# Kernel tuning notes

Measured on AMD Instinct MI355X. Metric: run time of the kernel, lower is better.

Reference implementation:

```python
import jax, jax.numpy as jnp
import numpy as np

HOPS = 3


def setup_inputs() -> dict:
    key = jax.random.key(0)
    ks = jax.random.split(key, 16)
    B, S, H, P = 8, 256, 768, 256
    N_E, N_T, N_R, T_TOK = 20000, 100000, 200, 4
    inv = H ** -0.5
    return {
        "last_hidden_state": jax.random.normal(ks[0], (B, S, H), jnp.float32),
        "attn_mask": jnp.ones((B, S), jnp.float32),
        "init_ent": jax.random.uniform(ks[1], (B, N_E), jnp.float32),
        "ents_embeds": jax.random.normal(ks[2], (N_E, T_TOK, H), jnp.float32) * 0.02,
        "W_q": jax.random.normal(ks[3], (H, P), jnp.float32) * inv,
        "W_v": jax.random.normal(ks[4], (H, P), jnp.float32) * inv,
        "W_p": jax.random.normal(ks[5], (P, 1), jnp.float32) * (P ** -0.5),
        "W_r": jax.random.normal(ks[6], (H, HOPS * N_R), jnp.float32) * inv,
        "W_c": jax.random.normal(ks[7], (H, HOPS * 2), jnp.float32) * inv,
        "L_w": jax.random.normal(ks[8], (H, H), jnp.float32) * inv,
        "heads": jax.random.randint(ks[9], (B, N_T), 0, N_E, jnp.int32),
        "rels": jax.random.randint(ks[10], (B, N_T), 0, N_R, jnp.int32),
        "tails": jax.random.randint(ks[11], (B, N_T), 0, N_E, jnp.int32),
    }


def reference(last_hidden_state, attn_mask, init_ent, ents_embeds,
              W_q, W_v, W_p, W_r, W_c, L_w, heads, rels, tails):
    B, S, H = last_hidden_state.shape
    N_E = init_ent.shape[1]

    # --- _pointer + _pointer_vecs: pointer attention over dialogue tokens ---
    D0 = last_hidden_state[:, -1, :]                                  # (B,H) last token = dialogue repr
    logits = (jnp.einsum('bh,hp->bp', D0, W_q)[:, None, :]
              + jnp.einsum('bsh,hp->bsp', last_hidden_state, W_v))    # (B,S,P)
    pointers = jax.nn.softmax(jnp.einsum('bsp,p->bs', logits, W_p[:, 0]), axis=1)
    D = jnp.sum(pointers[:, :, None] * last_hidden_state * attn_mask[:, :, None], axis=1)  # (B,H)

    # --- predict_rels / predict_checks ---
    rels_seq = jax.nn.softmax((D @ W_r).reshape(B, HOPS, -1), axis=2)    # (B,hops,N_R)
    checks_seq = jax.nn.softmax((D @ W_c).reshape(B, HOPS, -1), axis=2)  # (B,hops,2)

    # --- NEXT: per-batch per-hop sparse KG walk, one-hot sparse mm == gather/scatter ---
    def walk_one(e0, r_seq, h_idx, r_idx, t_idx):
        def hop(e, r):
            trip = r[r_idx] * e[h_idx]                                   # (N_T,) per-triple mass
            walked = jax.ops.segment_sum(trip, t_idx, num_segments=N_E)  # scatter to tails
            walked = walked / (walked.sum() + 1e-6)
            return walked, walked
        _, es = jax.lax.scan(hop, e0, r_seq)
        return es                                                        # (hops,N_E)

    walk = jax.vmap(walk_one)(init_ent, rels_seq, heads, rels, tails)    # (B,hops,N_E)

    # --- operates_on_checks: broadcasted matmul reduces to a single dot per (b,e) ---
    LD = D @ L_w                                                         # (B,H)
    scores = jnp.einsum('bh,eth->be', LD, ents_embeds)                   # (B,N_E)
    checks = jax.nn.softmax(walk * scores[:, None, :], axis=-1)          # (B,hops,N_E)

    # --- walk_or_check: mix walk vs check distribution per hop ---
    combined = jnp.stack([walk, checks], axis=2)                         # (B,hops,2,N_E)
    ents = jnp.einsum('bhc,bhce->bhe', checks_seq, combined)             # (B,hops,N_E)
    return ents
```

## Files before the change

### kernel.cpp

```cpp
#include <hip/hip_runtime.h>
#include <math.h>

#define NB 8
#define NS 256
#define NH 768
#define NE 20000
#define NT 100000

__device__ __forceinline__ float wsum(float v) {
#pragma unroll
  for (int off = 32; off; off >>= 1) v += __shfl_xor(v, off, 64);
  return v;
}
__device__ __forceinline__ float wmax(float v) {
#pragma unroll
  for (int off = 32; off; off >>= 1) v = fmaxf(v, __shfl_xor(v, off, 64));
  return v;
}

__global__ void k_prep(const float* __restrict__ Wv, const float* __restrict__ Wp,
                       float* __restrict__ wv) {
  int wave = threadIdx.x >> 6, lane = threadIdx.x & 63;
  int h = blockIdx.x * 4 + wave;
  const float4* Wv4 = (const float4*)Wv;
  const float4* Wp4 = (const float4*)Wp;
  float4 a = Wv4[h * 64 + lane];
  float4 p = Wp4[lane];
  float v = a.x * p.x + a.y * p.y + a.z * p.z + a.w * p.w;
  v = wsum(v);
  if (lane == 0) wv[h] = v;
}

__global__ void k_score(const float* __restrict__ lhs, const float* __restrict__ wv,
                        float* __restrict__ score) {
  int chunk = blockIdx.x, b = blockIdx.y;
  int wave = threadIdx.x >> 6, lane = threadIdx.x & 63;
  const float4* lhs4 = (const float4*)lhs;
  const float4* wv4 = (const float4*)wv;
  float4 w0 = wv4[lane], w1 = wv4[lane + 64], w2 = wv4[lane + 128];
#pragma unroll
  for (int i = 0; i < 8; i++) {
    int s = chunk * 32 + i * 4 + wave;
    const float4* row = lhs4 + (size_t)(b * NS + s) * 192;
    float4 a0 = row[lane], a1 = row[lane + 64], a2 = row[lane + 128];
    float v = a0.x * w0.x + a0.y * w0.y + a0.z * w0.z + a0.w * w0.w
            + a1.x * w1.x + a1.y * w1.y + a1.z * w1.z + a1.w * w1.w
            + a2.x * w2.x + a2.y * w2.y + a2.z * w2.z + a2.w * w2.w;
    v = wsum(v);
    if (lane == 0) score[b * NS + s] = v;
  }
}

__global__ void k_D(const float* __restrict__ lhs, const float* __restrict__ mask,
                    const float* __restrict__ score, float* __restrict__ Dv) {
  int b = blockIdx.x, chunk = blockIdx.y;
  int tid = threadIdx.x;
  __shared__ float red[256];
  __shared__ float pm[NS];
  float sv = score[b * NS + tid];
  red[tid] = sv; __syncthreads();
  for (int st = 128; st; st >>= 1) {
    if (tid < st) red[tid] = fmaxf(red[tid], red[tid + st]);
    __syncthreads();
  }
  float M = red[0]; __syncthreads();
  float e = expf(sv - M);
  red[tid] = e; __syncthreads();
  for (int st = 128; st; st >>= 1) {
    if (tid < st) red[tid] += red[tid + st];
    __syncthreads();
  }
  float Ssum = red[0];
  pm[tid] = (e / Ssum) * mask[b * NS + tid];
  __syncthreads();
  int h = chunk * 256 + tid;
  float acc = 0.f;
#pragma unroll 4
  for (int s = 0; s < NS; s++) acc += pm[s] * lhs[(size_t)(b * NS + s) * NH + h];
  Dv[b * NH + h] = acc;
}

__global__ void k_small(const float* __restrict__ Dv, const float* __restrict__ Wr,
                        const float* __restrict__ Wc, const float* __restrict__ Lw,
                        float* __restrict__ rels_raw, float* __restrict__ checks_raw,
                        float* __restrict__ LD) {
  __shared__ float Dl[NB * NH];
  __shared__ float part[4][64][8];
  int tid = threadIdx.x;
  for (int i = tid; i < NB * NH; i += 256) Dl[i] = Dv[i];
  __syncthreads();
  int c = tid & 63, q = tid >> 6;
  int C = blockIdx.x * 64 + c;
  const float* Wb = nullptr;
  float* outp = nullptr;
  int stride = 0, ostride = 0, col = 0;
  bool valid = (C < 1374);
  if (C < 600)      { Wb = Wr; stride = 600; col = C;       outp = rels_raw;   ostride = 600; }
  else if (C < 606) { Wb = Wc; stride = 6;   col = C - 600; outp = checks_raw; ostride = 6; }
  else if (valid)   { Wb = Lw; stride = 768; col = C - 606; outp = LD;         ostride = 768; }
  float p[8] = {0, 0, 0, 0, 0, 0, 0, 0};
  if (valid) {
    int h0 = q * 192;
    for (int h = h0; h < h0 + 192; h++) {
      float w = Wb[(size_t)h * stride + col];
#pragma unroll
      for (int b = 0; b < 8; b++) p[b] += Dl[b * NH + h] * w;
    }
  }
#pragma unroll
  for (int b = 0; b < 8; b++) part[q][c][b] = p[b];
  __syncthreads();
  if (q == 0 && valid) {
    for (int b = 0; b < 8; b++) {
      float v = part[0][c][b] + part[1][c][b] + part[2][c][b] + part[3][c][b];
      outp[b * ostride + col] = v;
    }
  }
}

__global__ void k_small2(float* __restrict__ rels, float* __restrict__ checks) {
  int b = blockIdx.x;
  int hop = threadIdx.x >> 6, lane = threadIdx.x & 63;
  float* r = rels + (size_t)(b * 3 + hop) * 200;
  float v0 = r[lane], v1 = r[lane + 64], v2 = r[lane + 128];
  float v3 = (lane < 8) ? r[lane + 192] : -INFINITY;
  float m = wmax(fmaxf(fmaxf(v0, v1), fmaxf(v2, v3)));
  float e0 = expf(v0 - m), e1 = expf(v1 - m), e2 = expf(v2 - m);
  float e3 = (lane < 8) ? expf(v3 - m) : 0.f;
  float s = wsum(e0 + e1 + e2 + e3);
  r[lane] = e0 / s; r[lane + 64] = e1 / s; r[lane + 128] = e2 / s;
  if (lane < 8) r[lane + 192] = e3 / s;
  if (lane == 0) {
    float* cc = checks + b * 6 + hop * 2;
    float c0 = cc[0], c1 = cc[1];
    float mm = fmaxf(c0, c1);
    float f0 = expf(c0 - mm), f1 = expf(c1 - mm);
    cc[0] = f0 / (f0 + f1); cc[1] = f1 / (f0 + f1);
  }
}

__global__ __launch_bounds__(256) void k_scores(const float* __restrict__ EE,
                                                const float* __restrict__ LD,
                                                float* __restrict__ scores) {
  int wave = threadIdx.x >> 6, lane = threadIdx.x & 63;
  int e = blockIdx.x * 4 + wave;
  const float4* EE4 = (const float4*)EE;
  const float4* LD4 = (const float4*)LD;
  float4 ld[3][8];
#pragma unroll
  for (int ph = 0; ph < 3; ph++)
#pragma unroll
    for (int b = 0; b < 8; b++) ld[ph][b] = LD4[b * 192 + ph * 64 + lane];
  float acc[8] = {0, 0, 0, 0, 0, 0, 0, 0};
  const float4* base = EE4 + (size_t)e * 768 + lane;
#pragma unroll
  for (int k = 0; k < 12; k++) {
    float4 v = base[k * 64];
    const int ph = k % 3;
#pragma unroll
    for (int b = 0; b < 8; b++)
      acc[b] += v.x * ld[ph][b].x + v.y * ld[ph][b].y + v.z * ld[ph][b].z + v.w * ld[ph][b].w;
  }
#pragma unroll
  for (int off = 32; off; off >>= 1)
#pragma unroll
    for (int b = 0; b < 8; b++) acc[b] += __shfl_xor(acc[b], off, 64);
  if (lane == 0) {
#pragma unroll
    for (int b = 0; b < 8; b++) scores[b * NE + e] = acc[b];
  }
}

__global__ void k_scatter(const int* __restrict__ heads, const int* __restrict__ rels,
                          const int* __restrict__ tails, const float* __restrict__ rels_seq,
                          const float* __restrict__ init_ent, const float* __restrict__ walk,
                          float* __restrict__ acc, int hop) {
  int t = blockIdx.x * 256 + threadIdx.x;
  if (t >= NB * NT) return;
  int b = t / NT;
  int hi = heads[t], ri = rels[t], ti = tails[t];
  float ev = (hop == 0) ? init_ent[(size_t)b * NE + hi]
                        : walk[((size_t)(b * 3) + hop - 1) * NE + hi];
  float rv = rels_seq[(size_t)(b * 3 + hop) * 200 + ri];
  atomicAdd(&acc[(size_t)b * NE + ti], rv * ev);
}

__global__ void k_norm(float* __restrict__ acc, float* __restrict__ walk, int hop) {
  int b = blockIdx.x, tid = threadIdx.x;
  float s = 0.f;
  for (int e = tid; e < NE; e += 1024) s += acc[(size_t)b * NE + e];
  s = wsum(s);
  __shared__ float red[16];
  __shared__ float stot;
  if ((tid & 63) == 0) red[tid >> 6] = s;
  __syncthreads();
  if (tid == 0) {
    float tt = 0.f;
    for (int i = 0; i < 16; i++) tt += red[i];
    stot = tt + 1e-6f;
  }
  __syncthreads();
  float denom = stot;
  float* w = walk + (size_t)(b * 3 + hop) * NE;
  for (int e = tid; e < NE; e += 1024) {
    w[e] = acc[(size_t)b * NE + e] / denom;
    acc[(size_t)b * NE + e] = 0.f;
  }
}

__global__ void k_final(const float* __restrict__ walk, const float* __restrict__ scores,
                        const float* __restrict__ checks_seq, float* __restrict__ out) {
  int row = blockIdx.x;
  int b = row / 3, hop = row % 3;
  const float* w = walk + (size_t)row * NE;
  const float* sc = scores + (size_t)b * NE;
  int tid = threadIdx.x;
  __shared__ float red[4];
  __shared__ float MM, SS;
  float m = -INFINITY;
  for (int e = tid; e < NE; e += 256) m = fmaxf(m, w[e] * sc[e]);
  m = wmax(m);
  if ((tid & 63) == 0) red[tid >> 6] = m;
  __syncthreads();
  if (tid == 0) MM = fmaxf(fmaxf(red[0], red[1]), fmaxf(red[2], red[3]));
  __syncthreads();
  float M = MM;
  float s = 0.f;
  for (int e = tid; e < NE; e += 256) s += expf(w[e] * sc[e] - M);
  s = wsum(s);
  if ((tid & 63) == 0) red[tid >> 6] = s;
  __syncthreads();
  if (tid == 0) SS = red[0] + red[1] + red[2] + red[3];
  __syncthreads();
  float Sv = SS;
  float cs0 = checks_seq[b * 6 + hop * 2 + 0];
  float cs1 = checks_seq[b * 6 + hop * 2 + 1];
  for (int e = tid; e < NE; e += 256) {
    float we = w[e];
    out[(size_t)row * NE + e] = cs0 * we + cs1 * (expf(we * sc[e] - M) / Sv);
  }
}

extern "C" void kernel_launch(void* const* d_in, const int* in_sizes, int n_in,
                              void* d_out, int out_size, void* d_ws, size_t ws_size,
                              hipStream_t stream) {
  const float* lhs      = (const float*)d_in[0];
  const float* mask     = (const float*)d_in[1];
  const float* init_ent = (const float*)d_in[2];
  const float* EE       = (const float*)d_in[3];
  const float* Wv       = (const float*)d_in[5];
  const float* Wp       = (const float*)d_in[6];
  const float* Wr       = (const float*)d_in[7];
  const float* Wc       = (const float*)d_in[8];
  const float* Lw       = (const float*)d_in[9];
  const int* heads      = (const int*)d_in[10];
  const int* rels       = (const int*)d_in[11];
  const int* tails      = (const int*)d_in[12];
  float* out = (float*)d_out;
  float* ws = (float*)d_ws;

  float* wv         = ws + 0;
  float* score      = ws + 768;
  float* Dv         = ws + 2816;
  float* LD         = ws + 8960;
  float* rels_seq   = ws + 15104;
  float* checks_seq = ws + 19904;
  float* scores     = ws + 19952;
  float* acc        = ws + 179952;
  float* walk       = ws + 339952;

  hipMemsetAsync(acc, 0, (size_t)NB * NE * sizeof(float), stream);
  k_prep<<<192, 256, 0, stream>>>(Wv, Wp, wv);
  k_score<<<dim3(8, NB), 256, 0, stream>>>(lhs, wv, score);
  k_D<<<dim3(NB, 3), 256, 0, stream>>>(lhs, mask, score, Dv);
  k_small<<<22, 256, 0, stream>>>(Dv, Wr, Wc, Lw, rels_seq, checks_seq, LD);
  k_small2<<<NB, 192, 0, stream>>>(rels_seq, checks_seq);
  k_scores<<<5000, 256, 0, stream>>>(EE, LD, scores);
  for (int hop = 0; hop < 3; hop++) {
    k_scatter<<<(NB * NT + 255) / 256, 256, 0, stream>>>(heads, rels, tails, rels_seq,
                                                         init_ent, walk, acc, hop);
    k_norm<<<NB, 1024, 0, stream>>>(acc, walk, hop);
  }
  k_final<<<NB * 3, 256, 0, stream>>>(walk, scores, checks_seq, out);
}
```

Baseline: 684.3 us.

## Fuse KG walk hops into one per-batch kernel with LDS atomics

Replaces the three scatter+normalize launch pairs and the global accumulator memset with a single kernel. Each of the 8 blocks holds its batch's 20000-entry accumulator in shared memory and runs all three hops with LDS atomics instead of global atomics. The pointer-softmax kernel now does its reduction with wave shuffles and splits the sequence sum across 4 thread groups, and the final softmax kernel uses 1024 threads per row. The walk now runs on only 8 workgroups, so the scatter has far less parallelism and relies on shared-memory atomics being fast enough to compensate.

```diff
diff --git a/kernel.cpp b/kernel.cpp
--- a/kernel.cpp
+++ b/kernel.cpp
@@ -51,33 +51,37 @@
   }
 }
 
-__global__ void k_D(const float* __restrict__ lhs, const float* __restrict__ mask,
-                    const float* __restrict__ score, float* __restrict__ Dv) {
+__global__ __launch_bounds__(1024) void k_D(const float* __restrict__ lhs,
+                                            const float* __restrict__ mask,
+                                            const float* __restrict__ score,
+                                            float* __restrict__ Dv) {
   int b = blockIdx.x, chunk = blockIdx.y;
   int tid = threadIdx.x;
-  __shared__ float red[256];
   __shared__ float pm[NS];
-  float sv = score[b * NS + tid];
-  red[tid] = sv; __syncthreads();
-  for (int st = 128; st; st >>= 1) {
-    if (tid < st) red[tid] = fmaxf(red[tid], red[tid + st]);
-    __syncthreads();
-  }
-  float M = red[0]; __syncthreads();
-  float e = expf(sv - M);
-  red[tid] = e; __syncthreads();
-  for (int st = 128; st; st >>= 1) {
-    if (tid < st) red[tid] += red[tid + st];
-    __syncthreads();
-  }
-  float Ssum = red[0];
-  pm[tid] = (e / Ssum) * mask[b * NS + tid];
-  __syncthreads();
-  int h = chunk * 256 + tid;
+  __shared__ float part[4][256];
+  if (tid < 64) {
+    int lane = tid;
+    float v0 = score[b * NS + lane], v1 = score[b * NS + lane + 64];
+    float v2 = score[b * NS + lane + 128], v3 = score[b * NS + lane + 192];
+    float m = wmax(fmaxf(fmaxf(v0, v1), fmaxf(v2, v3)));
+    float e0 = expf(v0 - m), e1 = expf(v1 - m), e2 = expf(v2 - m), e3 = expf(v3 - m);
+    float s = wsum(e0 + e1 + e2 + e3);
+    pm[lane] = e0 / s * mask[b * NS + lane];
+    pm[lane + 64] = e1 / s * mask[b * NS + lane + 64];
+    pm[lane + 128] = e2 / s * mask[b * NS + lane + 128];
+    pm[lane + 192] = e3 / s * mask[b * NS + lane + 192];
+  }
+  __syncthreads();
+  int g = tid >> 8;
+  int hh = tid & 255;
+  int h = chunk * 256 + hh;
   float acc = 0.f;
-#pragma unroll 4
-  for (int s = 0; s < NS; s++) acc += pm[s] * lhs[(size_t)(b * NS + s) * NH + h];
-  Dv[b * NH + h] = acc;
+  const float* base = lhs + (size_t)(b * NS + g * 64) * NH + h;
+#pragma unroll 8
+  for (int s = 0; s < 64; s++) acc += pm[g * 64 + s] * base[(size_t)s * NH];
+  part[g][hh] = acc;
+  __syncthreads();
+  if (g == 0) Dv[b * NH + h] = part[0][hh] + part[1][hh] + part[2][hh] + part[3][hh];
 }
 
 __global__ void k_small(const float* __restrict__ Dv, const float* __restrict__ Wr,
@@ -171,71 +175,94 @@
   }
 }
 
-__global__ void k_scatter(const int* __restrict__ heads, const int* __restrict__ rels,
-                          const int* __restrict__ tails, const float* __restrict__ rels_seq,
-                          const float* __restrict__ init_ent, const float* __restrict__ walk,
-                          float* __restrict__ acc, int hop) {
-  int t = blockIdx.x * 256 + threadIdx.x;
-  if (t >= NB * NT) return;
-  int b = t / NT;
-  int hi = heads[t], ri = rels[t], ti = tails[t];
-  float ev = (hop == 0) ? init_ent[(size_t)b * NE + hi]
-                        : walk[((size_t)(b * 3) + hop - 1) * NE + hi];
-  float rv = rels_seq[(size_t)(b * 3 + hop) * 200 + ri];
-  atomicAdd(&acc[(size_t)b * NE + ti], rv * ev);
-}
-
-__global__ void k_norm(float* __restrict__ acc, float* __restrict__ walk, int hop) {
-  int b = blockIdx.x, tid = threadIdx.x;
-  float s = 0.f;
-  for (int e = tid; e < NE; e += 1024) s += acc[(size_t)b * NE + e];
-  s = wsum(s);
+__global__ __launch_bounds__(1024) void k_walk(const int* __restrict__ heads,
+                                               const int* __restrict__ rels,
+                                               const int* __restrict__ tails,
+                                               const float* __restrict__ rels_seq,
+                                               const float* __restrict__ init_ent,
+                                               float* __restrict__ walk) {
+  int b = blockIdx.x;
+  int tid = threadIdx.x;
+  __shared__ float accs[NE];
   __shared__ float red[16];
   __shared__ float stot;
-  if ((tid & 63) == 0) red[tid >> 6] = s;
-  __syncthreads();
-  if (tid == 0) {
-    float tt = 0.f;
-    for (int i = 0; i < 16; i++) tt += red[i];
-    stot = tt + 1e-6f;
-  }
-  __syncthreads();
-  float denom = stot;
-  float* w = walk + (size_t)(b * 3 + hop) * NE;
-  for (int e = tid; e < NE; e += 1024) {
-    w[e] = acc[(size_t)b * NE + e] / denom;
-    acc[(size_t)b * NE + e] = 0.f;
-  }
-}
-
-__global__ void k_final(const float* __restrict__ walk, const float* __restrict__ scores,
-                        const float* __restrict__ checks_seq, float* __restrict__ out) {
+  for (int e = tid; e < NE; e += 1024) accs[e] = 0.f;
+  const int* hB = heads + (size_t)b * NT;
+  const int* rB = rels + (size_t)b * NT;
+  const int* tB = tails + (size_t)b * NT;
+  const float* src = init_ent + (size_t)b * NE;
+  __syncthreads();
+  for (int hop = 0; hop < 3; hop++) {
+    const float* rs = rels_seq + (size_t)(b * 3 + hop) * 200;
+    for (int t = tid; t < NT; t += 1024) {
+      float ev = src[hB[t]];
+      float rv = rs[rB[t]];
+      atomicAdd(&accs[tB[t]], rv * ev);
+    }
+    __syncthreads();
+    float s = 0.f;
+    for (int e = tid; e < NE; e += 1024) s += accs[e];
+    s = wsum(s);
+    if ((tid & 63) == 0) red[tid >> 6] = s;
+    __syncthreads();
+    if (tid == 0) {
+      float tt = 0.f;
+#pragma unroll
+      for (int i = 0; i < 16; i++) tt += red[i];
+      stot = tt + 1e-6f;
+    }
+    __syncthreads();
+    float denom = stot;
+    float* w = walk + (size_t)(b * 3 + hop) * NE;
+    for (int e = tid; e < NE; e += 1024) {
+      w[e] = accs[e] / denom;
+      accs[e] = 0.f;
+    }
+    src = w;
+    __syncthreads();
+  }
+}
+
+__global__ __launch_bounds__(1024) void k_final(const float* __restrict__ walk,
+                                                const float* __restrict__ scores,
+                                                const float* __restrict__ checks_seq,
+                                                float* __restrict__ out) {
   int row = blockIdx.x;
   int b = row / 3, hop = row % 3;
   const float* w = walk + (size_t)row * NE;
   const float* sc = scores + (size_t)b * NE;
   int tid = threadIdx.x;
-  __shared__ float red[4];
+  __shared__ float red[16];
   __shared__ float MM, SS;
   float m = -INFINITY;
-  for (int e = tid; e < NE; e += 256) m = fmaxf(m, w[e] * sc[e]);
+  for (int e = tid; e < NE; e += 1024) m = fmaxf(m, w[e] * sc[e]);
   m = wmax(m);
   if ((tid & 63) == 0) red[tid >> 6] = m;
   __syncthreads();
-  if (tid == 0) MM = fmaxf(fmaxf(red[0], red[1]), fmaxf(red[2], red[3]));
+  if (tid == 0) {
+    float mm = red[0];
+#pragma unroll
+    for (int i = 1; i < 16; i++) mm = fmaxf(mm, red[i]);
+    MM = mm;
+  }
   __syncthreads();
   float M = MM;
   float s = 0.f;
-  for (int e = tid; e < NE; e += 256) s += expf(w[e] * sc[e] - M);
+  for (int e = tid; e < NE; e += 1024) s += expf(w[e] * sc[e] - M);
   s = wsum(s);
   if ((tid & 63) == 0) red[tid >> 6] = s;
   __syncthreads();
-  if (tid == 0) SS = red[0] + red[1] + red[2] + red[3];
+  if (tid == 0) {
+    float tt = 0.f;
+#pragma unroll
+    for (int i = 0; i < 16; i++) tt += red[i];
+    SS = tt;
+  }
   __syncthreads();
   float Sv = SS;
   float cs0 = checks_seq[b * 6 + hop * 2 + 0];
   float cs1 = checks_seq[b * 6 + hop * 2 + 1];
-  for (int e = tid; e < NE; e += 256) {
+  for (int e = tid; e < NE; e += 1024) {
     float we = w[e];
     out[(size_t)row * NE + e] = cs0 * we + cs1 * (expf(we * sc[e] - M) / Sv);
   }
@@ -266,20 +293,14 @@
   float* rels_seq   = ws + 15104;
   float* checks_seq = ws + 19904;
   float* scores     = ws + 19952;
-  float* acc        = ws + 179952;
-  float* walk       = ws + 339952;
-
-  hipMemsetAsync(acc, 0, (size_t)NB * NE * sizeof(float), stream);
+  float* walk       = ws + 179952;
+
   k_prep<<<192, 256, 0, stream>>>(Wv, Wp, wv);
   k_score<<<dim3(8, NB), 256, 0, stream>>>(lhs, wv, score);
-  k_D<<<dim3(NB, 3), 256, 0, stream>>>(lhs, mask, score, Dv);
+  k_D<<<dim3(NB, 3), 1024, 0, stream>>>(lhs, mask, score, Dv);
   k_small<<<22, 256, 0, stream>>>(Dv, Wr, Wc, Lw, rels_seq, checks_seq, LD);
   k_small2<<<NB, 192, 0, stream>>>(rels_seq, checks_seq);
   k_scores<<<5000, 256, 0, stream>>>(EE, LD, scores);
-  for (int hop = 0; hop < 3; hop++) {
-    k_scatter<<<(NB * NT + 255) / 256, 256, 0, stream>>>(heads, rels, tails, rels_seq,
-                                                         init_ent, walk, acc, hop);
-    k_norm<<<NB, 1024, 0, stream>>>(acc, walk, hop);
-  }
-  k_final<<<NB * 3, 256, 0, stream>>>(walk, scores, checks_seq, out);
-}
+  k_walk<<<NB, 1024, 0, stream>>>(heads, rels, tails, rels_seq, init_ent, walk);
+  k_final<<<NB * 3, 1024, 0, stream>>>(walk, scores, checks_seq, out);
+}
```

Result: slower. 903.1 us (+32.0%).
